# Optimization experiments

Measured on AMD Instinct MI355X. Metric: run time of the kernel, lower is better.

The kernel has to match this reference:

```python
import jax, jax.numpy as jnp
import numpy as np

N = 50000      # nodes
E = 800000     # directed edges
IN = 128       # in_dim
H = 128        # hidden_dim
C = 16         # num_classes
G = 256        # num graphs in batch
EPS = 1e-5     # batchnorm eps


def setup_inputs() -> dict:
    key = jax.random.key(0)
    ks = jax.random.split(key, 12)
    x = jax.random.normal(ks[0], (N, IN), jnp.float32)
    edge_index = jax.random.randint(ks[1], (2, E), 0, N)
    batch = jnp.sort(jax.random.randint(ks[2], (N,), 0, G))
    scalar = jax.random.normal(ks[3], (G, 8), jnp.float32)
    # GCN layer params
    W0 = jax.random.normal(ks[4], (IN, H), jnp.float32) / np.sqrt(IN)
    b0 = jnp.zeros((H,), jnp.float32)
    Wk = jax.random.normal(ks[5], (2, H, H), jnp.float32) / np.sqrt(H)
    bk = jnp.zeros((2, H), jnp.float32)
    # BatchNorm (eval mode) params/buffers for 3 layers
    gamma = jnp.ones((3, H), jnp.float32)
    beta = jnp.zeros((3, H), jnp.float32)
    mean = jnp.zeros((3, H), jnp.float32)
    var = jnp.ones((3, H), jnp.float32)
    # scalar branch + classifier
    Ws = jax.random.normal(ks[6], (8, H // 2), jnp.float32) / np.sqrt(8.0)
    bs = jnp.zeros((H // 2,), jnp.float32)
    Wc1 = jax.random.normal(ks[7], (H + H // 2, H), jnp.float32) / np.sqrt(H + H // 2)
    bc1 = jnp.zeros((H,), jnp.float32)
    Wc2 = jax.random.normal(ks[8], (H, C), jnp.float32) / np.sqrt(H)
    bc2 = jnp.zeros((C,), jnp.float32)
    return {"x": x, "edge_index": edge_index, "batch": batch, "scalar": scalar,
            "W0": W0, "b0": b0, "Wk": Wk, "bk": bk,
            "gamma": gamma, "beta": beta, "mean": mean, "var": var,
            "Ws": Ws, "bs": bs, "Wc1": Wc1, "bc1": bc1, "Wc2": Wc2, "bc2": bc2}


def reference(x, edge_index, batch, scalar, W0, b0, Wk, bk,
              gamma, beta, mean, var, Ws, bs, Wc1, bc1, Wc2, bc2):
    n = x.shape[0]
    loop = jnp.arange(n)
    src = jnp.concatenate([edge_index[0], loop])  # add self-loops (PyG gcn_norm)
    dst = jnp.concatenate([edge_index[1], loop])
    deg = jax.ops.segment_sum(jnp.ones(src.shape[0], x.dtype), dst, num_segments=n)
    dinv = jax.lax.rsqrt(jnp.maximum(deg, 1.0))  # deg >= 1 because of self-loops
    norm = dinv[src] * dinv[dst]                 # symmetric normalization

    def gcn_bn_relu(h, W, b, g, be, m, v):
        h = h @ W                                   # [n, H] transform first (PyG GCNConv)
        msg = h[src] * norm[:, None]                # gather + normalize
        h = jax.ops.segment_sum(msg, dst, num_segments=n) + b  # scatter-add aggregate
        h = (h - m) * jax.lax.rsqrt(v + EPS) * g + be           # eval-mode BatchNorm
        return jax.nn.relu(h)                       # dropout is identity in eval

    h = gcn_bn_relu(x, W0, b0, gamma[0], beta[0], mean[0], var[0])
    for i in range(2):
        h = gcn_bn_relu(h, Wk[i], bk[i], gamma[i + 1], beta[i + 1], mean[i + 1], var[i + 1])

    # global mean pool over graphs
    counts = jax.ops.segment_sum(jnp.ones(n, x.dtype), batch, num_segments=G)
    gsum = jax.ops.segment_sum(h, batch, num_segments=G)
    gemb = gsum / jnp.maximum(counts, 1.0)[:, None]        # [G, H]

    semb = jax.nn.relu(scalar @ Ws + bs)                    # [G, H//2]
    z = jnp.concatenate([gemb, semb], axis=-1)              # [G, H + H//2]
    z = jax.nn.relu(z @ Wc1 + bc1)
    return z @ Wc2 + bc2                                    # [G, C]
```

## Files before the change

kernel.cpp:

```cpp
#include <hip/hip_runtime.h>
#include <hip/hip_bf16.h>

#define N_NODES 50000
#define N_EDGES 800000
#define DIM 128
#define N_GRAPHS 256
#define N_CLASSES 16
#define BN_EPS 1e-5f
#define NBUCKET 782
#define BIN_CHUNK 8192
#define BIN_BLOCKS ((N_EDGES + BIN_CHUNK - 1) / BIN_CHUNK)

typedef unsigned int uint;
typedef unsigned short ushort;
typedef __attribute__((ext_vector_type(8))) short short8;
typedef __attribute__((ext_vector_type(4))) float f32x4;

__device__ __forceinline__ ushort f32_to_bf16_rne(float f) {
    uint b = __float_as_uint(f);
    uint r = (b + 0x7fffu + ((b >> 16) & 1u)) >> 16;
    return (ushort)r;
}
__device__ __forceinline__ float bfx(uint r) { return __uint_as_float(r << 16); }
__device__ __forceinline__ float bfy(uint r) { return __uint_as_float(r & 0xffff0000u); }


__global__ void k_init(int* degcnt, float* gsum, float* counts) {
    int i = blockIdx.x * blockDim.x + threadIdx.x;
    if (i < N_NODES) degcnt[i] = 0;
    if (i < N_GRAPHS * DIM) gsum[i] = 0.f;
    if (i < N_GRAPHS) counts[i] = 0.f;
}

__global__ void k_count(const int* __restrict__ ei, int* __restrict__ degcnt) {
    int e = blockIdx.x * blockDim.x + threadIdx.x;
    if (e < N_EDGES) atomicAdd(&degcnt[ei[N_EDGES + e]], 1);
}

__global__ void k_dinv(const int* __restrict__ degcnt, float* __restrict__ dinv) {
    int v = blockIdx.x * blockDim.x + threadIdx.x;
    if (v < N_NODES) dinv[v] = rsqrtf((float)(degcnt[v] + 1));
}

__global__ __launch_bounds__(256) void k_bucketsum(const int* __restrict__ degcnt,
                                                   int* __restrict__ bucketcnt) {
    int wid = threadIdx.x >> 6, lane = threadIdx.x & 63;
    int gw = blockIdx.x * 4 + wid;
    int node = gw * 64 + lane;
    int c = (node < N_NODES) ? degcnt[node] : 0;
    #pragma unroll
    for (int off = 32; off; off >>= 1) c += __shfl_xor(c, off);
    if (lane == 0 && gw < NBUCKET) bucketcnt[gw] = c;
}

__device__ __forceinline__ int scan1024(int t, const int* __restrict__ in,
                                        int* o1, int* o2, int nE, int* wscr) {
    int e0 = t * 4;
    int v0 = (e0 + 0 < nE) ? in[e0 + 0] : 0;
    int v1 = (e0 + 1 < nE) ? in[e0 + 1] : 0;
    int v2 = (e0 + 2 < nE) ? in[e0 + 2] : 0;
    int v3 = (e0 + 3 < nE) ? in[e0 + 3] : 0;
    int s = v0 + v1 + v2 + v3;
    int lane = t & 63, wid = t >> 6;
    int incl = s;
    #pragma unroll
    for (int off = 1; off < 64; off <<= 1) {
        int nv = __shfl_up(incl, off);
        if (lane >= off) incl += nv;
    }
    if (lane == 63) wscr[wid] = incl;
    __syncthreads();
    int woff = 0;
    #pragma unroll
    for (int wj = 0; wj < 4; ++wj) if (wj < wid) woff += wscr[wj];
    int run = woff + incl - s;
    if (e0 + 0 < nE) { o1[e0 + 0] = run; o2[e0 + 0] = run; } run += v0;
    if (e0 + 1 < nE) { o1[e0 + 1] = run; o2[e0 + 1] = run; } run += v1;
    if (e0 + 2 < nE) { o1[e0 + 2] = run; o2[e0 + 2] = run; } run += v2;
    if (e0 + 3 < nE) { o1[e0 + 3] = run; o2[e0 + 3] = run; } run += v3;
    return run;
}

__global__ __launch_bounds__(256) void k_scanbuckets(const int* __restrict__ bucketcnt,
                                                     int* __restrict__ bucketbase,
                                                     int* __restrict__ bucketcur) {
    __shared__ int wsum[4];
    int t = threadIdx.x;
    int rend = scan1024(t, bucketcnt, bucketbase, bucketcur, NBUCKET, wsum);
    if (t == 255) bucketbase[NBUCKET] = rend;
}

__global__ __launch_bounds__(256) void k_bin(const int* __restrict__ ei,
                                             int* __restrict__ bucketcur,
                                             uint* __restrict__ staging) {
    __shared__ int hist[NBUCKET];
    __shared__ int lbase[NBUCKET];
    __shared__ int lcur[NBUCKET];
    __shared__ int gbase[NBUCKET];
    __shared__ uint sorted[BIN_CHUNK];
    __shared__ int wsum[4];
    int t = threadIdx.x;
    int e0 = blockIdx.x * BIN_CHUNK;
    int n = min(BIN_CHUNK, N_EDGES - e0);

    for (int i = t; i < NBUCKET; i += 256) hist[i] = 0;
    __syncthreads();
    for (int j = t; j < n; j += 256) {
        int d = ei[N_EDGES + e0 + j];
        atomicAdd(&hist[d >> 6], 1);
    }
    __syncthreads();
    scan1024(t, hist, lbase, lcur, NBUCKET, wsum);
    __syncthreads();
    for (int i = t; i < NBUCKET; i += 256) {
        int cnt = hist[i];
        if (cnt > 0) gbase[i] = atomicAdd(&bucketcur[i], cnt);
    }
    __syncthreads();
    for (int j = t; j < n; j += 256) {
        int s = ei[e0 + j];
        int d = ei[N_EDGES + e0 + j];
        int b = d >> 6;
        int loc = atomicAdd(&lcur[b], 1);
        sorted[loc] = (uint)s | ((uint)(d & 63) << 16) | ((uint)b << 22);
    }
    __syncthreads();
    for (int j = t; j < n; j += 256) {
        uint p = sorted[j];
        int b = (int)(p >> 22);
        staging[gbase[b] + (j - lbase[b])] = p;
    }
}

__global__ __launch_bounds__(256) void k_binfine(const uint* __restrict__ staging,
                                                 const int* __restrict__ bucketbase,
                                                 const int* __restrict__ degcnt,
                                                 int* __restrict__ rowptr,
                                                 int* __restrict__ colidx) {
    __shared__ int lcur[64];
    int t = threadIdx.x, b = blockIdx.x;
    int beg = bucketbase[b];
    int n = bucketbase[b + 1] - beg;
    int node0 = b * 64;

    if (t < 64) {
        int node = node0 + t;
        int c = (node < N_NODES) ? degcnt[node] : 0;
        int incl = c;
        #pragma unroll
        for (int off = 1; off < 64; off <<= 1) {
            int nv = __shfl_up(incl, off);
            if (t >= off) incl += nv;
        }
        int excl = incl - c;
        lcur[t] = excl;
        if (node < N_NODES) rowptr[node] = beg + excl;
    }
    if (b == 0 && t == 64) rowptr[N_NODES] = N_EDGES;
    __syncthreads();

    for (int j = t; j < n; j += 256) {
        uint p = staging[beg + j];
        int loc = atomicAdd(&lcur[(p >> 16) & 63u], 1);
        colidx[beg + loc] = (int)(p & 0xFFFFu);
    }
}

__global__ void k_bnfold(const float* __restrict__ b0, const float* __restrict__ bk,
                         const float* __restrict__ gamma, const float* __restrict__ beta,
                         const float* __restrict__ mean, const float* __restrict__ var,
                         float* __restrict__ alphaL, float* __restrict__ betaL) {
    int i = blockIdx.x * blockDim.x + threadIdx.x;
    if (i >= 3 * DIM) return;
    int l = i / DIM, c = i % DIM;
    float bias = (l == 0) ? b0[c] : bk[(l - 1) * DIM + c];
    float a = gamma[i] * rsqrtf(var[i] + BN_EPS);
    alphaL[i] = a;
    betaL[i] = (bias - mean[i]) * a + beta[i];
}

__global__ void k_wconv(const float* __restrict__ W0, const float* __restrict__ Wk,
                        ushort* __restrict__ Wt) {
    int i = blockIdx.x * blockDim.x + threadIdx.x;
    if (i >= 3 * DIM * DIM) return;
    int l = i >> 14, r = i & 16383, k = r >> 7, n = r & 127;
    float v = (l == 0) ? W0[k * DIM + n] : Wk[(l - 1) * DIM * DIM + k * DIM + n];
    Wt[l * DIM * DIM + n * DIM + k] = f32_to_bf16_rne(v);
}


#define GR 64
#define APITCH 136

union FragU { uint4 u; short8 s; };

__global__ __launch_bounds__(256) void k_gemm_mfma(const ushort* __restrict__ Abf,
                                                   const float* __restrict__ Af32,
                                                   const ushort* __restrict__ Wt,
                                                   const float* __restrict__ dinv,
                                                   ushort* __restrict__ out) {
    __shared__ ushort sA[GR * APITCH];
    __shared__ ushort sW[DIM * APITCH];
    int t = threadIdx.x;
    int base = blockIdx.x * GR;

    #pragma unroll
    for (int it = 0; it < 8; ++it) {
        int q = it * 256 + t;
        int n = q >> 4, c = q & 15;
        *(uint4*)&sW[n * APITCH + c * 8] = *(const uint4*)&Wt[n * DIM + c * 8];
    }
    if (Af32) {
        #pragma unroll
        for (int it = 0; it < 8; ++it) {
            int q = it * 256 + t;
            int row = q >> 5, c = q & 31;
            int gr = base + row;
            float4 v = make_float4(0.f, 0.f, 0.f, 0.f);
            if (gr < N_NODES) v = *(const float4*)&Af32[(size_t)gr * DIM + c * 4];
            ushort pk[4] = {f32_to_bf16_rne(v.x), f32_to_bf16_rne(v.y),
                            f32_to_bf16_rne(v.z), f32_to_bf16_rne(v.w)};
            *(uint2*)&sA[row * APITCH + c * 4] = *(const uint2*)pk;
        }
    } else {
        #pragma unroll
        for (int it = 0; it < 4; ++it) {
            int q = it * 256 + t;
            int row = q >> 4, c = q & 15;
            int gr = base + row;
            uint4 v = make_uint4(0u, 0u, 0u, 0u);
            if (gr < N_NODES) v = *(const uint4*)&Abf[(size_t)gr * DIM + c * 8];
            *(uint4*)&sA[row * APITCH + c * 8] = v;
        }
    }
    __syncthreads();

    int w = t >> 6, lane = t & 63;
    int lm = lane & 15, lg = lane >> 4;

    f32x4 acc[8];
    #pragma unroll
    for (int nt = 0; nt < 8; ++nt) acc[nt] = (f32x4){0.f, 0.f, 0.f, 0.f};

    const ushort* aRow = &sA[(w * 16 + lm) * APITCH];
    #pragma unroll
    for (int kc = 0; kc < 4; ++kc) {
        int ko = kc * 32 + lg * 8;
        FragU au; au.u = *(const uint4*)&aRow[ko];
        #pragma unroll
        for (int nt = 0; nt < 8; ++nt) {
            FragU bu; bu.u = *(const uint4*)&sW[(nt * 16 + lm) * APITCH + ko];
            acc[nt] = __builtin_amdgcn_mfma_f32_16x16x32_bf16(au.s, bu.s, acc[nt], 0, 0, 0);
        }
    }

    int m0 = base + w * 16 + lg * 4;
    float dv[4];
    #pragma unroll
    for (int j = 0; j < 4; ++j) {
        int gr = m0 + j;
        dv[j] = (gr < N_NODES) ? dinv[gr] : 0.f;
    }
    #pragma unroll
    for (int nt = 0; nt < 8; ++nt) {
        int n = nt * 16 + lm;
        #pragma unroll
        for (int j = 0; j < 4; ++j) {
            int gr = m0 + j;
            if (gr < N_NODES)
                out[(size_t)gr * DIM + n] = f32_to_bf16_rne(acc[nt][j] * dv[j]);
        }
    }
}


__global__ __launch_bounds__(256) void k_aggregate(const ushort* __restrict__ hs,
                                                   const int* __restrict__ rowptr,
                                                   const int* __restrict__ colidx,
                                                   const float* __restrict__ dinv,
                                                   const float* __restrict__ alpha,
                                                   const float* __restrict__ beta,
                                                   ushort* __restrict__ out) {
    int v = blockIdx.x * 4 + (threadIdx.x >> 6);
    if (v >= N_NODES) return;
    int lane = threadIdx.x & 63;
    int c = 2 * lane;

    uint selfr = *(const uint*)&hs[(size_t)v * DIM + c];
    float ax = bfx(selfr), ay = bfy(selfr);

    int beg = rowptr[v], end = rowptr[v + 1];
    int i = beg;
    for (; i + 4 <= end; i += 4) {
        int u0 = colidx[i], u1 = colidx[i + 1], u2 = colidx[i + 2], u3 = colidx[i + 3];
        uint b0 = *(const uint*)&hs[(size_t)u0 * DIM + c];
        uint b1 = *(const uint*)&hs[(size_t)u1 * DIM + c];
        uint b2 = *(const uint*)&hs[(size_t)u2 * DIM + c];
        uint b3 = *(const uint*)&hs[(size_t)u3 * DIM + c];
        ax += bfx(b0) + bfx(b1) + bfx(b2) + bfx(b3);
        ay += bfy(b0) + bfy(b1) + bfy(b2) + bfy(b3);
    }
    for (; i < end; ++i) {
        int u = colidx[i];
        uint b = *(const uint*)&hs[(size_t)u * DIM + c];
        ax += bfx(b); ay += bfy(b);
    }

    float dvv = dinv[v];
    float2 al = *(const float2*)&alpha[c];
    float2 be = *(const float2*)&beta[c];
    float ox = fmaxf(fmaf(ax * dvv, al.x, be.x), 0.f);
    float oy = fmaxf(fmaf(ay * dvv, al.y, be.y), 0.f);
    uint lo = f32_to_bf16_rne(ox), hi = f32_to_bf16_rne(oy);
    *(uint*)&out[(size_t)v * DIM + c] = lo | (hi << 16);
}


#define POOL_CH 16
__global__ __launch_bounds__(256) void k_pool(const ushort* __restrict__ h,
                                              const int* __restrict__ batch,
                                              float* __restrict__ gsum,
                                              float* __restrict__ counts) {
    int wv = blockIdx.x * 4 + (threadIdx.x >> 6);
    int n0 = wv * POOL_CH;
    if (n0 >= N_NODES) return;
    int n1 = min(n0 + POOL_CH, N_NODES);
    int lane = threadIdx.x & 63;
    int c = 2 * lane;

    float ax = 0.f, ay = 0.f;
    int cnt = 0;
    int gcur = batch[n0];
    for (int n = n0; n < n1; ++n) {
        int g = batch[n];
        if (g != gcur) {
            atomicAdd(&gsum[gcur * DIM + c], ax);
            atomicAdd(&gsum[gcur * DIM + c + 1], ay);
            if (lane == 0) atomicAdd(&counts[gcur], (float)cnt);
            ax = ay = 0.f; cnt = 0; gcur = g;
        }
        uint hv = *(const uint*)&h[(size_t)n * DIM + c];
        ax += bfx(hv); ay += bfy(hv); cnt++;
    }
    atomicAdd(&gsum[gcur * DIM + c], ax);
    atomicAdd(&gsum[gcur * DIM + c + 1], ay);
    if (lane == 0) atomicAdd(&counts[gcur], (float)cnt);
}


__global__ __launch_bounds__(128) void k_head(const float* __restrict__ gsum,
                                              const float* __restrict__ counts,
                                              const float* __restrict__ scalar,
                                              const float* __restrict__ Ws, const float* __restrict__ bs,
                                              const float* __restrict__ Wc1, const float* __restrict__ bc1,
                                              const float* __restrict__ Wc2, const float* __restrict__ bc2,
                                              float* __restrict__ out) {
    __shared__ float z[DIM + DIM / 2];
    __shared__ float z1[DIM];
    int g = blockIdx.x, t = threadIdx.x;

    float cntv = fmaxf(counts[g], 1.0f);
    z[t] = gsum[g * DIM + t] / cntv;
    if (t < DIM / 2) {
        float s = bs[t];
        #pragma unroll
        for (int i = 0; i < 8; ++i) s = fmaf(scalar[g * 8 + i], Ws[i * (DIM / 2) + t], s);
        z[DIM + t] = fmaxf(s, 0.f);
    }
    __syncthreads();

    {
        float s = bc1[t];
        for (int i = 0; i < DIM + DIM / 2; ++i) s = fmaf(z[i], Wc1[i * DIM + t], s);
        z1[t] = fmaxf(s, 0.f);
    }
    __syncthreads();

    if (t < N_CLASSES) {
        float s = bc2[t];
        for (int i = 0; i < DIM; ++i) s = fmaf(z1[i], Wc2[i * N_CLASSES + t], s);
        out[g * N_CLASSES + t] = s;
    }
}


extern "C" void kernel_launch(void* const* d_in, const int* in_sizes, int n_in,
                              void* d_out, int out_size, void* d_ws, size_t ws_size,
                              hipStream_t stream) {
    const float* x      = (const float*)d_in[0];
    const int*   ei     = (const int*)d_in[1];
    const int*   batch  = (const int*)d_in[2];
    const float* scalar = (const float*)d_in[3];
    const float* W0     = (const float*)d_in[4];
    const float* b0     = (const float*)d_in[5];
    const float* Wk     = (const float*)d_in[6];
    const float* bk     = (const float*)d_in[7];
    const float* gamma  = (const float*)d_in[8];
    const float* beta   = (const float*)d_in[9];
    const float* mean   = (const float*)d_in[10];
    const float* var    = (const float*)d_in[11];
    const float* Ws     = (const float*)d_in[12];
    const float* bs     = (const float*)d_in[13];
    const float* Wc1    = (const float*)d_in[14];
    const float* bc1    = (const float*)d_in[15];
    const float* Wc2    = (const float*)d_in[16];
    const float* bc2    = (const float*)d_in[17];
    float* out = (float*)d_out;

    char* p = (char*)d_ws;
    auto alloc = [&](size_t bytes) -> void* {
        void* r = (void*)p;
        p += (bytes + 255) & ~(size_t)255;
        return r;
    };
    float*  dinv      = (float*)alloc((size_t)N_NODES * 4);
    int*    degcnt    = (int*)  alloc((size_t)N_NODES * 4);
    int*    bucketcnt = (int*)  alloc((size_t)NBUCKET * 4);
    int*    bucketbase= (int*)  alloc(((size_t)NBUCKET + 1) * 4);
    int*    bucketcur = (int*)  alloc((size_t)NBUCKET * 4);
    uint*   staging   = (uint*) alloc((size_t)N_EDGES * 4);
    int*    rowptr    = (int*)  alloc(((size_t)N_NODES + 1) * 4);
    int*    colidx    = (int*)  alloc((size_t)N_EDGES * 4);
    float*  alphaL    = (float*)alloc(3 * DIM * 4);
    float*  betaL     = (float*)alloc(3 * DIM * 4);
    float*  gsum      = (float*)alloc((size_t)N_GRAPHS * DIM * 4);
    float*  counts    = (float*)alloc((size_t)N_GRAPHS * 4);
    ushort* Wt        = (ushort*)alloc((size_t)3 * DIM * DIM * 2);
    ushort* bufAct    = (ushort*)alloc((size_t)N_NODES * DIM * 2);
    ushort* bufH      = (ushort*)alloc((size_t)N_NODES * DIM * 2);

    const int edgeBlocks = (N_EDGES + 255) / 256;
    const int nodeBlocks = (N_NODES + 255) / 256;
    const int gemmBlocks = (N_NODES + GR - 1) / GR;
    const int aggBlocks  = (N_NODES + 3) / 4;
    const int poolWaves  = (N_NODES + POOL_CH - 1) / POOL_CH;
    const int poolBlocks = (poolWaves + 3) / 4;

    k_init<<<nodeBlocks, 256, 0, stream>>>(degcnt, gsum, counts);
    k_count<<<edgeBlocks, 256, 0, stream>>>(ei, degcnt);
    k_dinv<<<nodeBlocks, 256, 0, stream>>>(degcnt, dinv);
    k_bucketsum<<<(NBUCKET + 3) / 4, 256, 0, stream>>>(degcnt, bucketcnt);
    k_scanbuckets<<<1, 256, 0, stream>>>(bucketcnt, bucketbase, bucketcur);
    k_bin<<<BIN_BLOCKS, 256, 0, stream>>>(ei, bucketcur, staging);
    k_binfine<<<NBUCKET, 256, 0, stream>>>(staging, bucketbase, degcnt, rowptr, colidx);
    k_bnfold<<<2, 256, 0, stream>>>(b0, bk, gamma, beta, mean, var, alphaL, betaL);
    k_wconv<<<192, 256, 0, stream>>>(W0, Wk, Wt);

    k_gemm_mfma<<<gemmBlocks, 256, 0, stream>>>(nullptr, x, Wt, dinv, bufH);
    k_aggregate<<<aggBlocks, 256, 0, stream>>>(bufH, rowptr, colidx, dinv,
                                               alphaL + 0 * DIM, betaL + 0 * DIM, bufAct);
    k_gemm_mfma<<<gemmBlocks, 256, 0, stream>>>(bufAct, nullptr, Wt + DIM * DIM, dinv, bufH);
    k_aggregate<<<aggBlocks, 256, 0, stream>>>(bufH, rowptr, colidx, dinv,
                                               alphaL + 1 * DIM, betaL + 1 * DIM, bufAct);
    k_gemm_mfma<<<gemmBlocks, 256, 0, stream>>>(bufAct, nullptr, Wt + 2 * DIM * DIM, dinv, bufH);
    k_aggregate<<<aggBlocks, 256, 0, stream>>>(bufH, rowptr, colidx, dinv,
                                               alphaL + 2 * DIM, betaL + 2 * DIM, bufAct);

    k_pool<<<poolBlocks, 256, 0, stream>>>(bufAct, batch, gsum, counts);
    k_head<<<N_GRAPHS, 128, 0, stream>>>(gsum, counts, scalar, Ws, bs, Wc1, bc1, Wc2, bc2, out);
}
```

Before: 372.9 us.

## Derive degrees from bucket histograms and fuse mean pooling into head

Replaces the per-edge global-atomic degree count, the dinv kernel and the bucket-sum kernel with a shared-memory bucket histogram. Per-node degree and dinv are now computed inside the fine binning kernel from the staged edges. Global mean pooling no longer uses atomics: graph ranges are found from the sorted batch vector, and the head kernel sums each graph's rows directly. This removes several launches and the global atomic contention, but the head now does a serial per-graph reduction with only 256 blocks.

```diff
diff --git a/kernel.cpp b/kernel.cpp
--- a/kernel.cpp
+++ b/kernel.cpp
@@ -25,32 +25,36 @@
 __device__ __forceinline__ float bfy(uint r) { return __uint_as_float(r & 0xffff0000u); }
 
 
-__global__ void k_init(int* degcnt, float* gsum, float* counts) {
+__global__ void k_init(int* bucketcnt, int* gstart, int* gend) {
     int i = blockIdx.x * blockDim.x + threadIdx.x;
-    if (i < N_NODES) degcnt[i] = 0;
-    if (i < N_GRAPHS * DIM) gsum[i] = 0.f;
-    if (i < N_GRAPHS) counts[i] = 0.f;
-}
-
-__global__ void k_count(const int* __restrict__ ei, int* __restrict__ degcnt) {
-    int e = blockIdx.x * blockDim.x + threadIdx.x;
-    if (e < N_EDGES) atomicAdd(&degcnt[ei[N_EDGES + e]], 1);
-}
-
-__global__ void k_dinv(const int* __restrict__ degcnt, float* __restrict__ dinv) {
-    int v = blockIdx.x * blockDim.x + threadIdx.x;
-    if (v < N_NODES) dinv[v] = rsqrtf((float)(degcnt[v] + 1));
-}
-
-__global__ __launch_bounds__(256) void k_bucketsum(const int* __restrict__ degcnt,
-                                                   int* __restrict__ bucketcnt) {
-    int wid = threadIdx.x >> 6, lane = threadIdx.x & 63;
-    int gw = blockIdx.x * 4 + wid;
-    int node = gw * 64 + lane;
-    int c = (node < N_NODES) ? degcnt[node] : 0;
-    #pragma unroll
-    for (int off = 32; off; off >>= 1) c += __shfl_xor(c, off);
-    if (lane == 0 && gw < NBUCKET) bucketcnt[gw] = c;
+    if (i < NBUCKET) bucketcnt[i] = 0;
+    if (i < N_GRAPHS) { gstart[i] = N_NODES; gend[i] = 0; }
+}
+
+__global__ void k_ranges(const int* __restrict__ batch,
+                         int* __restrict__ gstart, int* __restrict__ gend) {
+    int i = blockIdx.x * blockDim.x + threadIdx.x;
+    if (i >= N_NODES) return;
+    int b = batch[i];
+    if (i == 0 || batch[i - 1] != b) atomicMin(&gstart[b], i);
+    if (i == N_NODES - 1 || batch[i + 1] != b) atomicMax(&gend[b], i + 1);
+}
+
+__global__ __launch_bounds__(256) void k_binhist(const int* __restrict__ ei,
+                                                 int* __restrict__ bucketcnt) {
+    __shared__ int hist[NBUCKET];
+    int t = threadIdx.x;
+    int e0 = blockIdx.x * BIN_CHUNK;
+    int n = min(BIN_CHUNK, N_EDGES - e0);
+    for (int i = t; i < NBUCKET; i += 256) hist[i] = 0;
+    __syncthreads();
+    for (int j = t; j < n; j += 256) {
+        int d = ei[N_EDGES + e0 + j];
+        atomicAdd(&hist[d >> 6], 1);
+    }
+    __syncthreads();
+    for (int i = t; i < NBUCKET; i += 256)
+        if (hist[i] > 0) atomicAdd(&bucketcnt[i], hist[i]);
 }
 
 __device__ __forceinline__ int scan1024(int t, const int* __restrict__ in,
@@ -134,25 +138,33 @@
 
 __global__ __launch_bounds__(256) void k_binfine(const uint* __restrict__ staging,
                                                  const int* __restrict__ bucketbase,
-                                                 const int* __restrict__ degcnt,
+                                                 float* __restrict__ dinv,
                                                  int* __restrict__ rowptr,
                                                  int* __restrict__ colidx) {
+    __shared__ int hist64[64];
     __shared__ int lcur[64];
     int t = threadIdx.x, b = blockIdx.x;
     int beg = bucketbase[b];
     int n = bucketbase[b + 1] - beg;
     int node0 = b * 64;
 
+    if (t < 64) hist64[t] = 0;
+    __syncthreads();
+    for (int j = t; j < n; j += 256)
+        atomicAdd(&hist64[(staging[beg + j] >> 16) & 63u], 1);
+    __syncthreads();
+
     if (t < 64) {
+        int deg = hist64[t];
         int node = node0 + t;
-        int c = (node < N_NODES) ? degcnt[node] : 0;
-        int incl = c;
+        if (node < N_NODES) dinv[node] = rsqrtf((float)(deg + 1));
+        int incl = deg;
         #pragma unroll
         for (int off = 1; off < 64; off <<= 1) {
             int nv = __shfl_up(incl, off);
             if (t >= off) incl += nv;
         }
-        int excl = incl - c;
+        int excl = incl - deg;
         lcur[t] = excl;
         if (node < N_NODES) rowptr[node] = beg + excl;
     }
@@ -316,40 +328,9 @@
 }
 
 
-#define POOL_CH 16
-__global__ __launch_bounds__(256) void k_pool(const ushort* __restrict__ h,
-                                              const int* __restrict__ batch,
-                                              float* __restrict__ gsum,
-                                              float* __restrict__ counts) {
-    int wv = blockIdx.x * 4 + (threadIdx.x >> 6);
-    int n0 = wv * POOL_CH;
-    if (n0 >= N_NODES) return;
-    int n1 = min(n0 + POOL_CH, N_NODES);
-    int lane = threadIdx.x & 63;
-    int c = 2 * lane;
-
-    float ax = 0.f, ay = 0.f;
-    int cnt = 0;
-    int gcur = batch[n0];
-    for (int n = n0; n < n1; ++n) {
-        int g = batch[n];
-        if (g != gcur) {
-            atomicAdd(&gsum[gcur * DIM + c], ax);
-            atomicAdd(&gsum[gcur * DIM + c + 1], ay);
-            if (lane == 0) atomicAdd(&counts[gcur], (float)cnt);
-            ax = ay = 0.f; cnt = 0; gcur = g;
-        }
-        uint hv = *(const uint*)&h[(size_t)n * DIM + c];
-        ax += bfx(hv); ay += bfy(hv); cnt++;
-    }
-    atomicAdd(&gsum[gcur * DIM + c], ax);
-    atomicAdd(&gsum[gcur * DIM + c + 1], ay);
-    if (lane == 0) atomicAdd(&counts[gcur], (float)cnt);
-}
-
-
-__global__ __launch_bounds__(128) void k_head(const float* __restrict__ gsum,
-                                              const float* __restrict__ counts,
+__global__ __launch_bounds__(128) void k_head(const ushort* __restrict__ h,
+                                              const int* __restrict__ gstart,
+                                              const int* __restrict__ gend,
                                               const float* __restrict__ scalar,
                                               const float* __restrict__ Ws, const float* __restrict__ bs,
                                               const float* __restrict__ Wc1, const float* __restrict__ bc1,
@@ -359,8 +340,21 @@
     __shared__ float z1[DIM];
     int g = blockIdx.x, t = threadIdx.x;
 
-    float cntv = fmaxf(counts[g], 1.0f);
-    z[t] = gsum[g * DIM + t] / cntv;
+    int s0 = gstart[g], s1 = gend[g];
+    float sum = 0.f;
+    int n = s0;
+    for (; n + 4 <= s1; n += 4) {
+        float a0 = __uint_as_float((uint)h[(size_t)(n + 0) * DIM + t] << 16);
+        float a1 = __uint_as_float((uint)h[(size_t)(n + 1) * DIM + t] << 16);
+        float a2 = __uint_as_float((uint)h[(size_t)(n + 2) * DIM + t] << 16);
+        float a3 = __uint_as_float((uint)h[(size_t)(n + 3) * DIM + t] << 16);
+        sum += a0 + a1 + a2 + a3;
+    }
+    for (; n < s1; ++n)
+        sum += __uint_as_float((uint)h[(size_t)n * DIM + t] << 16);
+    float cnt = (float)((s1 > s0) ? (s1 - s0) : 1);
+    z[t] = sum / cnt;
+
     if (t < DIM / 2) {
         float s = bs[t];
         #pragma unroll
@@ -414,35 +408,30 @@
         return r;
     };
     float*  dinv      = (float*)alloc((size_t)N_NODES * 4);
-    int*    degcnt    = (int*)  alloc((size_t)N_NODES * 4);
     int*    bucketcnt = (int*)  alloc((size_t)NBUCKET * 4);
     int*    bucketbase= (int*)  alloc(((size_t)NBUCKET + 1) * 4);
     int*    bucketcur = (int*)  alloc((size_t)NBUCKET * 4);
     uint*   staging   = (uint*) alloc((size_t)N_EDGES * 4);
     int*    rowptr    = (int*)  alloc(((size_t)N_NODES + 1) * 4);
     int*    colidx    = (int*)  alloc((size_t)N_EDGES * 4);
+    int*    gstart    = (int*)  alloc((size_t)N_GRAPHS * 4);
+    int*    gend      = (int*)  alloc((size_t)N_GRAPHS * 4);
     float*  alphaL    = (float*)alloc(3 * DIM * 4);
     float*  betaL     = (float*)alloc(3 * DIM * 4);
-    float*  gsum      = (float*)alloc((size_t)N_GRAPHS * DIM * 4);
-    float*  counts    = (float*)alloc((size_t)N_GRAPHS * 4);
     ushort* Wt        = (ushort*)alloc((size_t)3 * DIM * DIM * 2);
     ushort* bufAct    = (ushort*)alloc((size_t)N_NODES * DIM * 2);
     ushort* bufH      = (ushort*)alloc((size_t)N_NODES * DIM * 2);
 
-    const int edgeBlocks = (N_EDGES + 255) / 256;
     const int nodeBlocks = (N_NODES + 255) / 256;
     const int gemmBlocks = (N_NODES + GR - 1) / GR;
     const int aggBlocks  = (N_NODES + 3) / 4;
-    const int poolWaves  = (N_NODES + POOL_CH - 1) / POOL_CH;
-    const int poolBlocks = (poolWaves + 3) / 4;
-
-    k_init<<<nodeBlocks, 256, 0, stream>>>(degcnt, gsum, counts);
-    k_count<<<edgeBlocks, 256, 0, stream>>>(ei, degcnt);
-    k_dinv<<<nodeBlocks, 256, 0, stream>>>(degcnt, dinv);
-    k_bucketsum<<<(NBUCKET + 3) / 4, 256, 0, stream>>>(degcnt, bucketcnt);
+
+    k_init<<<(NBUCKET + 255) / 256, 256, 0, stream>>>(bucketcnt, gstart, gend);
+    k_ranges<<<nodeBlocks, 256, 0, stream>>>(batch, gstart, gend);
+    k_binhist<<<BIN_BLOCKS, 256, 0, stream>>>(ei, bucketcnt);
     k_scanbuckets<<<1, 256, 0, stream>>>(bucketcnt, bucketbase, bucketcur);
     k_bin<<<BIN_BLOCKS, 256, 0, stream>>>(ei, bucketcur, staging);
-    k_binfine<<<NBUCKET, 256, 0, stream>>>(staging, bucketbase, degcnt, rowptr, colidx);
+    k_binfine<<<NBUCKET, 256, 0, stream>>>(staging, bucketbase, dinv, rowptr, colidx);
     k_bnfold<<<2, 256, 0, stream>>>(b0, bk, gamma, beta, mean, var, alphaL, betaL);
     k_wconv<<<192, 256, 0, stream>>>(W0, Wk, Wt);
 
@@ -456,6 +445,6 @@
     k_aggregate<<<aggBlocks, 256, 0, stream>>>(bufH, rowptr, colidx, dinv,
                                                alphaL + 2 * DIM, betaL + 2 * DIM, bufAct);
 
-    k_pool<<<poolBlocks, 256, 0, stream>>>(bufAct, batch, gsum, counts);
-    k_head<<<N_GRAPHS, 128, 0, stream>>>(gsum, counts, scalar, Ws, bs, Wc1, bc1, Wc2, bc2, out);
-}
+    k_head<<<N_GRAPHS, 128, 0, stream>>>(bufAct, gstart, gend, scalar,
+                                         Ws, bs, Wc1, bc1, Wc2, bc2, out);
+}
```

Result: faster. 342.8 us (-8.1%).
